# Kernel tuning notes

Measured on AMD Instinct MI355X. Metric: run time of the kernel, lower is better.

Reference implementation:

```python
import jax, jax.numpy as jnp
import numpy as np

B, Tx, H, E, Ky = 64, 128, 1024, 512, 32000


def setup_inputs() -> dict:
    key = jax.random.key(0)
    ks = jax.random.split(key, 14)
    s = 0.02
    return {
        "input": jax.random.randint(ks[0], (B,), 0, Ky),
        "hidden": jax.random.normal(ks[1], (B, H), jnp.float32),
        "enc_output": jax.random.normal(ks[2], (Tx, B, 2 * H), jnp.float32),
        # learned params
        "emb_W": jax.random.normal(ks[3], (Ky, E), jnp.float32) * s,
        "Wih": jax.random.normal(ks[4], (3 * H, E + 2 * H), jnp.float32) * s,
        "Whh": jax.random.normal(ks[5], (3 * H, H), jnp.float32) * s,
        "bih": jax.random.normal(ks[6], (3 * H,), jnp.float32) * s,
        "bhh": jax.random.normal(ks[7], (3 * H,), jnp.float32) * s,
        "lsm_W": jax.random.normal(ks[8], (Ky, 3 * H), jnp.float32) * s,
        "lsm_b": jax.random.normal(ks[9], (Ky,), jnp.float32) * s,
        "aW1": jax.random.normal(ks[10], (H, 3 * H), jnp.float32) * s,
        "ab1": jax.random.normal(ks[11], (H,), jnp.float32) * s,
        "aW2": jax.random.normal(ks[12], (1, H), jnp.float32) * s,
        "ab2": jax.random.normal(ks[13], (1,), jnp.float32) * s,
    }


def _alignment(hidden, enc_output, aW1, ab1, aW2, ab2):
    # hidden [B,H] broadcast over Tx; attn_input [Tx,B,3H]
    Tx_ = enc_output.shape[0]
    h_rep = jnp.broadcast_to(hidden[None], (Tx_,) + hidden.shape)
    attn_in = jnp.concatenate([h_rep, enc_output], axis=2)
    a = jnp.tanh(jnp.einsum('tbi,hi->tbh', attn_in, aW1) + ab1)
    score = jnp.einsum('tbh,oh->tbo', a, aW2) + ab2   # [Tx,B,1]
    w = jax.nn.softmax(score, axis=0)                 # softmax over Tx (dim=0)
    # context = sum_t w[t,b] * enc_output[t,b,:]  -> [B,2H]
    context = jnp.einsum('tb,tbk->bk', w[..., 0], enc_output)
    return context


def _gru_cell(x, h, Wih, Whh, bih, bhh):
    gi = x @ Wih.T + bih   # [B,3H]
    gh = h @ Whh.T + bhh   # [B,3H]
    Hd = h.shape[1]
    i_r, i_z, i_n = gi[:, :Hd], gi[:, Hd:2 * Hd], gi[:, 2 * Hd:]
    h_r, h_z, h_n = gh[:, :Hd], gh[:, Hd:2 * Hd], gh[:, 2 * Hd:]
    r = jax.nn.sigmoid(i_r + h_r)
    z = jax.nn.sigmoid(i_z + h_z)
    n = jnp.tanh(i_n + r * h_n)
    return (1.0 - z) * n + z * h


def reference(input, hidden, enc_output, emb_W, Wih, Whh, bih, bhh,
              lsm_W, lsm_b, aW1, ab1, aW2, ab2):
    context = _alignment(hidden, enc_output, aW1, ab1, aW2, ab2)  # [B,2H]
    embed = emb_W[input]                                          # [B,E]
    rnn_in = jnp.concatenate([embed, context], axis=1)            # [B,E+2H]
    h_new = _gru_cell(rnn_in, hidden, Wih, Whh, bih, bhh)         # [B,H]
    logits = jnp.concatenate([h_new, context], axis=1) @ lsm_W.T + lsm_b
    output = jax.nn.log_softmax(logits, axis=-1)                  # [B,Ky]
    return output, h_new
```

## Files before the change

kernel.cpp:

```cpp
#include <hip/hip_runtime.h>
#include <hip/hip_bf16.h>

#define B_  64
#define TX  128
#define H_  1024
#define E_  512
#define KY  32000
#define H2  2048
#define H3  3072
#define EC  2560
#define M_  (TX*B_)
#define WST 132
#define NS  4

typedef __bf16 bf16x8 __attribute__((ext_vector_type(8)));
typedef unsigned short u16x8 __attribute__((ext_vector_type(8)));
typedef float f32x4 __attribute__((ext_vector_type(4)));

__device__ __forceinline__ unsigned short f2bf(float f) {
  unsigned int u = __builtin_bit_cast(unsigned int, f);
  u += 0x7fff + ((u >> 16) & 1);
  return (unsigned short)(u >> 16);
}

__device__ __forceinline__ void gload16(const void* g, void* l) {
  __builtin_amdgcn_global_load_lds(
      (const __attribute__((address_space(1))) unsigned int*)g,
      (__attribute__((address_space(3))) unsigned int*)l, 16, 0, 0);
}

__global__ void kc_all(const float* __restrict__ enc, const float* __restrict__ aW1,
                       const float* __restrict__ hidden,
                       unsigned short* __restrict__ encb, unsigned short* __restrict__ w1b,
                       unsigned short* __restrict__ hb) {
  size_t gid = (size_t)blockIdx.x * 256 + threadIdx.x;
  if (gid < 2097152) {
    size_t i = gid * 8;
    float4 v0 = *(const float4*)(enc + i);
    float4 v1 = *(const float4*)(enc + i + 4);
    u16x8 o;
    o[0]=f2bf(v0.x); o[1]=f2bf(v0.y); o[2]=f2bf(v0.z); o[3]=f2bf(v0.w);
    o[4]=f2bf(v1.x); o[5]=f2bf(v1.y); o[6]=f2bf(v1.z); o[7]=f2bf(v1.w);
    *(u16x8*)(encb + i) = o;
  } else if (gid < 2359296) {
    size_t idx = (gid - 2097152) * 8;
    int row = (int)(idx >> 11);
    int col = (int)(idx & 2047);
    const float* s = aW1 + (size_t)row * H3 + H_ + col;
    float4 v0 = *(const float4*)(s);
    float4 v1 = *(const float4*)(s + 4);
    u16x8 o;
    o[0]=f2bf(v0.x); o[1]=f2bf(v0.y); o[2]=f2bf(v0.z); o[3]=f2bf(v0.w);
    o[4]=f2bf(v1.x); o[5]=f2bf(v1.y); o[6]=f2bf(v1.z); o[7]=f2bf(v1.w);
    *(u16x8*)(w1b + idx) = o;
  } else {
    size_t idx = (gid - 2359296) * 8;
    if (idx < 65536) {
      float4 v0 = *(const float4*)(hidden + idx);
      float4 v1 = *(const float4*)(hidden + idx + 4);
      u16x8 o;
      o[0]=f2bf(v0.x); o[1]=f2bf(v0.y); o[2]=f2bf(v0.z); o[3]=f2bf(v0.w);
      o[4]=f2bf(v1.x); o[5]=f2bf(v1.y); o[6]=f2bf(v1.z); o[7]=f2bf(v1.w);
      *(u16x8*)(hb + idx) = o;
    }
  }
}

__global__ void k1_hpart(const float* __restrict__ hidden, const float* __restrict__ aW1,
                         const float* __restrict__ ab1, float* __restrict__ hpart) {
  int b = blockIdx.y;
  int wave = threadIdx.x >> 6;
  int lane = threadIdx.x & 63;
  int h = blockIdx.x * 4 + wave;
  const float* wrow = aW1 + (size_t)h * H3;
  const float* hrow = hidden + b * H_;
  float acc = 0.f;
  for (int j = 0; j < H_ / 64; ++j) {
    int i = j * 64 + lane;
    acc += hrow[i] * wrow[i];
  }
  for (int off = 32; off; off >>= 1) acc += __shfl_down(acc, off);
  if (lane == 0) hpart[b * H_ + h] = acc + ab1[h];
}

__global__ __launch_bounds__(256) void k2_mfma(
    const unsigned short* __restrict__ encb, const unsigned short* __restrict__ w1b,
    const float* __restrict__ hpart, const float* __restrict__ aW2,
    float* __restrict__ scorepart) {
  __shared__ __align__(16) unsigned short As[128 * 64];
  __shared__ __align__(16) unsigned short Bs[128 * 64];
  __shared__ float red[128][2];
  int wg = blockIdx.x;
  int swz = (wg & 7) * 64 + (wg >> 3);
  int mt = swz >> 3, nt = swz & 7;
  int m0 = mt * 128, n0 = nt * 128;
  int tid = threadIdx.x;
  int lane = tid & 63, wid = tid >> 6;
  int wr = wid >> 1, wc = wid & 1;
  f32x4 z = {0.f, 0.f, 0.f, 0.f};
  f32x4 acc[4][4];
  #pragma unroll
  for (int i = 0; i < 4; ++i)
    #pragma unroll
    for (int j = 0; j < 4; ++j) acc[i][j] = z;

  int srow = lane >> 3;
  int scol = ((lane & 7) ^ srow) * 8;
  for (int k0 = 0; k0 < H2; k0 += 64) {
    __syncthreads();
    #pragma unroll
    for (int i = 0; i < 4; ++i) {
      int ci = wid * 4 + i;
      int row = ci * 8 + srow;
      gload16(&encb[(size_t)(m0 + row) * H2 + k0 + scol], &As[ci * 512]);
      gload16(&w1b [(size_t)(n0 + row) * H2 + k0 + scol], &Bs[ci * 512]);
    }
    __syncthreads();
    #pragma unroll
    for (int ks = 0; ks < 2; ++ks) {
      bf16x8 af[4], bfr[4];
      #pragma unroll
      for (int i = 0; i < 4; ++i) {
        int ra = wr * 64 + i * 16 + (lane & 15);
        int rb = wc * 64 + i * 16 + (lane & 15);
        int og = (ks * 4 + (lane >> 4));
        af[i]  = *(const bf16x8*)&As[ra * 64 + ((og ^ (ra & 7)) * 8)];
        bfr[i] = *(const bf16x8*)&Bs[rb * 64 + ((og ^ (rb & 7)) * 8)];
      }
      #pragma unroll
      for (int mi = 0; mi < 4; ++mi)
        #pragma unroll
        for (int ni = 0; ni < 4; ++ni)
          acc[mi][ni] = __builtin_amdgcn_mfma_f32_16x16x32_bf16(af[mi], bfr[ni], acc[mi][ni], 0, 0, 0);
    }
  }
  int q = lane >> 4, c = lane & 15;
  #pragma unroll
  for (int mi = 0; mi < 4; ++mi) {
    #pragma unroll
    for (int r = 0; r < 4; ++r) {
      int mloc = wr * 64 + mi * 16 + q * 4 + r;
      int b = (mi * 16 + q * 4 + r) & 63;
      float p = 0.f;
      #pragma unroll
      for (int ni = 0; ni < 4; ++ni) {
        int n = n0 + wc * 64 + ni * 16 + c;
        p += aW2[n] * tanhf(hpart[b * H_ + n] + acc[mi][ni][r]);
      }
      p += __shfl_xor(p, 1); p += __shfl_xor(p, 2);
      p += __shfl_xor(p, 4); p += __shfl_xor(p, 8);
      if (c == 0) red[mloc][wc] = p;
    }
  }
  __syncthreads();
  if (tid < 128)
    scorepart[(size_t)nt * M_ + m0 + tid] = red[tid][0] + red[tid][1];
}

__global__ __launch_bounds__(256) void k2_gemm_score(
    const float* __restrict__ enc, const float* __restrict__ aW1,
    const float* __restrict__ hpart, const float* __restrict__ aW2,
    float* __restrict__ scorepart) {
  __shared__ float As[32][68];
  __shared__ float Bs[32][68];
  __shared__ float red[64][17];
  int m0 = blockIdx.x * 64;
  int n0 = blockIdx.y * 64;
  int tid = threadIdx.x;
  int ty = tid >> 4, tx = tid & 15;
  float acc[4][4] = {};
  for (int k0 = 0; k0 < H2; k0 += 32) {
    #pragma unroll
    for (int l = 0; l < 2; ++l) {
      int fi = tid + l * 256;
      int m = fi >> 3;
      int kq = (fi & 7) * 4;
      const float4 v = *(const float4*)&enc[(size_t)(m0 + m) * H2 + k0 + kq];
      As[kq + 0][m] = v.x; As[kq + 1][m] = v.y; As[kq + 2][m] = v.z; As[kq + 3][m] = v.w;
      const float4 u = *(const float4*)&aW1[(size_t)(n0 + m) * H3 + H_ + k0 + kq];
      Bs[kq + 0][m] = u.x; Bs[kq + 1][m] = u.y; Bs[kq + 2][m] = u.z; Bs[kq + 3][m] = u.w;
    }
    __syncthreads();
    #pragma unroll
    for (int kk = 0; kk < 32; ++kk) {
      float4 av = *(const float4*)&As[kk][ty * 4];
      float4 bv = *(const float4*)&Bs[kk][tx * 4];
      float a[4] = {av.x, av.y, av.z, av.w};
      float b[4] = {bv.x, bv.y, bv.z, bv.w};
      #pragma unroll
      for (int i = 0; i < 4; ++i)
        #pragma unroll
        for (int j = 0; j < 4; ++j)
          acc[i][j] += a[i] * b[j];
    }
    __syncthreads();
  }
  #pragma unroll
  for (int i = 0; i < 4; ++i) {
    int m = m0 + ty * 4 + i;
    int bb = m & 63;
    float p = 0.f;
    #pragma unroll
    for (int j = 0; j < 4; ++j) {
      int n = n0 + tx * 4 + j;
      p += aW2[n] * tanhf(hpart[bb * H_ + n] + acc[i][j]);
    }
    red[ty * 4 + i][tx] = p;
  }
  __syncthreads();
  if (tid < 64) {
    float s = 0.f;
    #pragma unroll
    for (int j = 0; j < 16; ++j) s += red[tid][j];
    scorepart[(size_t)blockIdx.y * M_ + m0 + tid] = s;
  }
}

__global__ void k3_softmax(const float* __restrict__ scorepart, const float* __restrict__ ab2,
                           float* __restrict__ w, int nb) {
  int b = blockIdx.x;
  int t = threadIdx.x;
  float s = ab2[0];
  for (int k = 0; k < nb; ++k) s += scorepart[k * M_ + t * B_ + b];
  __shared__ float sm[128];
  sm[t] = s; __syncthreads();
  for (int off = 64; off; off >>= 1) {
    if (t < off) sm[t] = fmaxf(sm[t], sm[t + off]);
    __syncthreads();
  }
  float mx = sm[0]; __syncthreads();
  float e = expf(s - mx);
  sm[t] = e; __syncthreads();
  for (int off = 64; off; off >>= 1) {
    if (t < off) sm[t] += sm[t + off];
    __syncthreads();
  }
  w[t * B_ + b] = e / sm[0];
}

__global__ __launch_bounds__(256) void k4c_ctx(
    const unsigned short* __restrict__ encb, const float* __restrict__ scorepart,
    const float* __restrict__ ab2, const int* __restrict__ input,
    const float* __restrict__ emb_W, unsigned short* __restrict__ rb,
    unsigned short* __restrict__ xb) {
  int b = blockIdx.y;
  if (blockIdx.x == 4) {
    int tok = input[b];
    for (int c = threadIdx.x; c < E_; c += 256)
      rb[b * EC + c] = f2bf(emb_W[(size_t)tok * E_ + c]);
    return;
  }
  int t = threadIdx.x;
  __shared__ float wl[TX];
  __shared__ float sm[TX];
  float s = 0.f;
  if (t < TX) {
    s = ab2[0];
    #pragma unroll
    for (int k = 0; k < 8; ++k) s += scorepart[k * M_ + t * B_ + b];
    sm[t] = s;
  }
  __syncthreads();
  for (int off = 64; off; off >>= 1) {
    if (t < off) sm[t] = fmaxf(sm[t], sm[t + off]);
    __syncthreads();
  }
  float mx = sm[0]; __syncthreads();
  float e = 0.f;
  if (t < TX) { e = expf(s - mx); sm[t] = e; }
  __syncthreads();
  for (int off = 64; off; off >>= 1) {
    if (t < off) sm[t] += sm[t + off];
    __syncthreads();
  }
  if (t < TX) wl[t] = e / sm[0];
  __syncthreads();

  int kp = blockIdx.x * 256 + threadIdx.x;
  float a0 = 0.f, a1 = 0.f;
  for (int tt = 0; tt < TX; ++tt) {
    unsigned int u = *(const unsigned int*)&encb[((size_t)tt * B_ + b) * H2 + kp * 2];
    float e0 = __builtin_bit_cast(float, u << 16);
    float e1 = __builtin_bit_cast(float, u & 0xffff0000u);
    float wt = wl[tt];
    a0 += wt * e0; a1 += wt * e1;
  }
  unsigned int ob = (unsigned int)f2bf(a0) | ((unsigned int)f2bf(a1) << 16);
  *(unsigned int*)&rb[b * EC + E_ + kp * 2] = ob;
  *(unsigned int*)&xb[b * H3 + H_ + kp * 2] = ob;
}

__global__ void k4_context(const float* __restrict__ enc, const float* __restrict__ w,
                           float* __restrict__ context) {
  int b = blockIdx.y;
  int k = blockIdx.x * 256 + threadIdx.x;
  __shared__ float wl[TX];
  if (threadIdx.x < TX) wl[threadIdx.x] = w[threadIdx.x * B_ + b];
  __syncthreads();
  float acc = 0.f;
  for (int t = 0; t < TX; ++t)
    acc += wl[t] * enc[((size_t)t * B_ + b) * H2 + k];
  context[b * H2 + k] = acc;
}
__global__ void k5a_rnnin(const int* __restrict__ input, const float* __restrict__ emb_W,
                          const float* __restrict__ context, float* __restrict__ rnn_in) {
  int b = blockIdx.x;
  int tok = input[b];
  for (int c = threadIdx.x; c < EC; c += blockDim.x)
    rnn_in[b * EC + c] = (c < E_) ? emb_W[(size_t)tok * E_ + c] : context[b * H2 + (c - E_)];
}

__device__ __forceinline__ void gemmT_body(const float* __restrict__ x,
    const float* __restrict__ W, int lda, const float* __restrict__ bias,
    float* __restrict__ po, int N, int K, int kbeg, int kend, bool addb,
    float* __restrict__ Ws) {
  int tid = threadIdx.x;
  int b = tid & 63, g = tid >> 6;
  int n0 = blockIdx.x * 64;
  float acc[16] = {};
  const float4* xv = (const float4*)(x + (size_t)b * K);
  for (int k0 = kbeg; k0 < kend; k0 += 128) {
    __syncthreads();
    #pragma unroll
    for (int l = 0; l < 8; ++l) {
      int f = l * 256 + tid;
      int row = f >> 5, c4 = f & 31;
      float4 v = *(const float4*)&W[(size_t)(n0 + row) * lda + k0 + c4 * 4];
      *(float4*)&Ws[row * WST + c4 * 4] = v;
    }
    __syncthreads();
    #pragma unroll
    for (int kb = 0; kb < 128; kb += 16) {
      float4 x0 = xv[(k0 + kb) / 4 + 0];
      float4 x1 = xv[(k0 + kb) / 4 + 1];
      float4 x2 = xv[(k0 + kb) / 4 + 2];
      float4 x3 = xv[(k0 + kb) / 4 + 3];
      #pragma unroll
      for (int i = 0; i < 16; ++i) {
        const float* wr = &Ws[(g * 16 + i) * WST + kb];
        float4 w0 = *(const float4*)(wr + 0);
        float4 w1 = *(const float4*)(wr + 4);
        float4 w2 = *(const float4*)(wr + 8);
        float4 w3 = *(const float4*)(wr + 12);
        acc[i] += x0.x*w0.x + x0.y*w0.y + x0.z*w0.z + x0.w*w0.w
                + x1.x*w1.x + x1.y*w1.y + x1.z*w1.z + x1.w*w1.w
                + x2.x*w2.x + x2.y*w2.y + x2.z*w2.z + x2.w*w2.w
                + x3.x*w3.x + x3.y*w3.y + x3.z*w3.z + x3.w*w3.w;
      }
    }
  }
  #pragma unroll
  for (int i = 0; i < 16; ++i) {
    int n = n0 + g * 16 + i;
    float v = acc[i];
    if (addb) v += bias[n];
    po[(size_t)b * N + n] = v;
  }
}

__global__ __launch_bounds__(256) void k_gemm_T(
    const float* __restrict__ x, const float* __restrict__ W,
    const float* __restrict__ bias, float* __restrict__ out, int N, int K) {
  __shared__ float Ws[64 * WST];
  int ks = blockIdx.y;
  int kchunk = K / gridDim.y;
  gemmT_body(x, W, K, bias, out + (size_t)ks * 64 * N, N, K, ks * kchunk, ks * kchunk + kchunk, ks == 0, Ws);
}

__global__ __launch_bounds__(256) void k_gates_mfma(
    const unsigned short* __restrict__ rb, const unsigned short* __restrict__ hb,
    const float* __restrict__ Wih, const float* __restrict__ Whh,
    const float* __restrict__ bih, const float* __restrict__ bhh,
    float* __restrict__ gi, float* __restrict__ gh) {
  __shared__ __align__(16) float Ws[64 * 128];
  __shared__ __align__(16) unsigned short Xs[64 * 128];
  int tid = threadIdx.x;
  int wv = tid >> 6, lane = tid & 63;
  int r = lane & 15, kg = lane >> 4;
  int n0 = blockIdx.x * 64;
  int n = n0 + wv * 16 + r;
  int s = blockIdx.y;
  const float* W; const unsigned short* x; const float* bias;
  float* po; int lda, kbase, KC; bool addb;
  if (s < 2) { W = Wih; x = rb; lda = EC; kbase = s * 1280; KC = 1280;
               po = gi + (size_t)s * B_ * H3; bias = bih; addb = (s == 0); }
  else       { W = Whh; x = hb; lda = H_; kbase = 0; KC = 1024;
               po = gh; bias = bhh; addb = true; }
  f32x4 a0 = {0.f, 0.f, 0.f, 0.f}, a1 = a0, a2 = a0, a3 = a0;

  for (int ch = 0; ch < KC; ch += 128) {
    __syncthreads();
    #pragma unroll
    for (int i = 0; i < 8; ++i) {
      int rowW = (wv * 8 + i) * 2 + (lane >> 5);
      int sc = (lane & 31) ^ (rowW & 15);
      gload16(&W[(size_t)(n0 + rowW) * lda + kbase + ch + sc * 4],
              &Ws[(wv * 8 + i) * 256]);
    }
    #pragma unroll
    for (int i = 0; i < 4; ++i) {
      int rowX = (wv * 4 + i) * 4 + (lane >> 4);
      int sc = (lane & 15) ^ (rowX & 15);
      gload16(&x[(size_t)rowX * lda + kbase + ch + sc * 8],
              &Xs[(wv * 4 + i) * 512]);
    }
    __syncthreads();
    #pragma unroll
    for (int ss = 0; ss < 4; ++ss) {
      int uw0 = (ss * 8 + kg * 2) ^ r;
      int uw1 = (ss * 8 + kg * 2 + 1) ^ r;
      int rw = wv * 16 + r;
      float4 wa = *(const float4*)&Ws[rw * 128 + uw0 * 4];
      float4 wb = *(const float4*)&Ws[rw * 128 + uw1 * 4];
      u16x8 bu;
      bu[0] = f2bf(wa.x); bu[1] = f2bf(wa.y); bu[2] = f2bf(wa.z); bu[3] = f2bf(wa.w);
      bu[4] = f2bf(wb.x); bu[5] = f2bf(wb.y); bu[6] = f2bf(wb.z); bu[7] = f2bf(wb.w);
      bf16x8 bf = __builtin_bit_cast(bf16x8, bu);
      int ux = (ss * 4 + kg) ^ r;
      u16x8 x0 = *(const u16x8*)&Xs[(r)      * 128 + ux * 8];
      u16x8 x1 = *(const u16x8*)&Xs[(16 + r) * 128 + ux * 8];
      u16x8 x2 = *(const u16x8*)&Xs[(32 + r) * 128 + ux * 8];
      u16x8 x3 = *(const u16x8*)&Xs[(48 + r) * 128 + ux * 8];
      a0 = __builtin_amdgcn_mfma_f32_16x16x32_bf16(__builtin_bit_cast(bf16x8, x0), bf, a0, 0, 0, 0);
      a1 = __builtin_amdgcn_mfma_f32_16x16x32_bf16(__builtin_bit_cast(bf16x8, x1), bf, a1, 0, 0, 0);
      a2 = __builtin_amdgcn_mfma_f32_16x16x32_bf16(__builtin_bit_cast(bf16x8, x2), bf, a2, 0, 0, 0);
      a3 = __builtin_amdgcn_mfma_f32_16x16x32_bf16(__builtin_bit_cast(bf16x8, x3), bf, a3, 0, 0, 0);
    }
  }
  float bv = addb ? bias[n] : 0.f;
  int r0 = kg * 4;
  #pragma unroll
  for (int rr = 0; rr < 4; ++rr) {
    po[(size_t)(r0 + rr) * H3 + n]      = a0[rr] + bv;
    po[(size_t)(16 + r0 + rr) * H3 + n] = a1[rr] + bv;
    po[(size_t)(32 + r0 + rr) * H3 + n] = a2[rr] + bv;
    po[(size_t)(48 + r0 + rr) * H3 + n] = a3[rr] + bv;
  }
}

__global__ void k5c_gates(const float* __restrict__ gip, const float* __restrict__ ghp,
                          int gis, int ghs, int do_ctx,
                          const float* __restrict__ hidden, const float* __restrict__ context,
                          float* __restrict__ hnew_out, unsigned short* __restrict__ xb) {
  int b = blockIdx.x;
  for (int h = threadIdx.x; h < H_; h += blockDim.x) {
    float ir = 0.f, iz = 0.f, inn = 0.f;
    for (int s = 0; s < gis; ++s) {
      const float* gb = gip + (size_t)s * B_ * H3 + (size_t)b * H3;
      ir += gb[h]; iz += gb[H_ + h]; inn += gb[H2 + h];
    }
    float hr = 0.f, hz = 0.f, hn = 0.f;
    for (int s = 0; s < ghs; ++s) {
      const float* gb = ghp + (size_t)s * B_ * H3 + (size_t)b * H3;
      hr += gb[h]; hz += gb[H_ + h]; hn += gb[H2 + h];
    }
    float r = 1.f / (1.f + expf(-(ir + hr)));
    float z = 1.f / (1.f + expf(-(iz + hz)));
    float n = tanhf(inn + r * hn);
    float hv = hidden[b * H_ + h];
    float hnew = (1.f - z) * n + z * hv;
    hnew_out[b * H_ + h] = hnew;
    xb[b * H3 + h] = f2bf(hnew);
  }
  if (do_ctx)
    for (int c = threadIdx.x; c < H2; c += blockDim.x)
      xb[b * H3 + H_ + c] = f2bf(context[b * H2 + c]);
}

__device__ __forceinline__ void k6_stage(float4 wa, float4 wb,
    const unsigned short* __restrict__ xp, int off,
    f32x4& a0, f32x4& a1, f32x4& a2, f32x4& a3) {
  u16x8 bu;
  bu[0] = f2bf(wa.x); bu[1] = f2bf(wa.y); bu[2] = f2bf(wa.z); bu[3] = f2bf(wa.w);
  bu[4] = f2bf(wb.x); bu[5] = f2bf(wb.y); bu[6] = f2bf(wb.z); bu[7] = f2bf(wb.w);
  bf16x8 bf = __builtin_bit_cast(bf16x8, bu);
  u16x8 x0 = *(const u16x8*)(xp + off);
  u16x8 x1 = *(const u16x8*)(xp + 16 * H3 + off);
  u16x8 x2 = *(const u16x8*)(xp + 32 * H3 + off);
  u16x8 x3 = *(const u16x8*)(xp + 48 * H3 + off);
  a0 = __builtin_amdgcn_mfma_f32_16x16x32_bf16(__builtin_bit_cast(bf16x8, x0), bf, a0, 0, 0, 0);
  a1 = __builtin_amdgcn_mfma_f32_16x16x32_bf16(__builtin_bit_cast(bf16x8, x1), bf, a1, 0, 0, 0);
  a2 = __builtin_amdgcn_mfma_f32_16x16x32_bf16(__builtin_bit_cast(bf16x8, x2), bf, a2, 0, 0, 0);
  a3 = __builtin_amdgcn_mfma_f32_16x16x32_bf16(__builtin_bit_cast(bf16x8, x3), bf, a3, 0, 0, 0);
}

__global__ __launch_bounds__(256) void k6_split(
    const unsigned short* __restrict__ xb, const float* __restrict__ W,
    float* __restrict__ part) {
  __shared__ __align__(16) float Ws[64 * 128];
  __shared__ __align__(16) unsigned short Xs[64 * 128];
  int tid = threadIdx.x;
  int wv = tid >> 6, lane = tid & 63;
  int r = lane & 15, kg = lane >> 4;
  int n = blockIdx.x * 64 + wv * 16 + r;
  int ks = blockIdx.y;
  const int KC = H3 / NS;
  int kbase = ks * KC;
  f32x4 a0 = {0.f, 0.f, 0.f, 0.f}, a1 = a0, a2 = a0, a3 = a0;

  for (int ch = 0; ch < KC; ch += 128) {
    __syncthreads();
    #pragma unroll
    for (int i = 0; i < 8; ++i) {
      int rowW = (wv * 8 + i) * 2 + (lane >> 5);
      int sc = (lane & 31) ^ (rowW & 15);
      gload16(&W[(size_t)(blockIdx.x * 64 + rowW) * H3 + kbase + ch + sc * 4],
              &Ws[(wv * 8 + i) * 256]);
    }
    #pragma unroll
    for (int i = 0; i < 4; ++i) {
      int rowX = (wv * 4 + i) * 4 + (lane >> 4);
      int sc = (lane & 15) ^ (rowX & 15);
      gload16(&xb[(size_t)rowX * H3 + kbase + ch + sc * 8],
              &Xs[(wv * 4 + i) * 512]);
    }
    __syncthreads();
    #pragma unroll
    for (int s = 0; s < 4; ++s) {
      int uw0 = (s * 8 + kg * 2) ^ r;
      int uw1 = (s * 8 + kg * 2 + 1) ^ r;
      int rw = wv * 16 + r;
      float4 wa = *(const float4*)&Ws[rw * 128 + uw0 * 4];
      float4 wb = *(const float4*)&Ws[rw * 128 + uw1 * 4];
      u16x8 bu;
      bu[0] = f2bf(wa.x); bu[1] = f2bf(wa.y); bu[2] = f2bf(wa.z); bu[3] = f2bf(wa.w);
      bu[4] = f2bf(wb.x); bu[5] = f2bf(wb.y); bu[6] = f2bf(wb.z); bu[7] = f2bf(wb.w);
      bf16x8 bf = __builtin_bit_cast(bf16x8, bu);
      int ux = (s * 4 + kg) ^ r;
      u16x8 x0 = *(const u16x8*)&Xs[(r)      * 128 + ux * 8];
      u16x8 x1 = *(const u16x8*)&Xs[(16 + r) * 128 + ux * 8];
      u16x8 x2 = *(const u16x8*)&Xs[(32 + r) * 128 + ux * 8];
      u16x8 x3 = *(const u16x8*)&Xs[(48 + r) * 128 + ux * 8];
      a0 = __builtin_amdgcn_mfma_f32_16x16x32_bf16(__builtin_bit_cast(bf16x8, x0), bf, a0, 0, 0, 0);
      a1 = __builtin_amdgcn_mfma_f32_16x16x32_bf16(__builtin_bit_cast(bf16x8, x1), bf, a1, 0, 0, 0);
      a2 = __builtin_amdgcn_mfma_f32_16x16x32_bf16(__builtin_bit_cast(bf16x8, x2), bf, a2, 0, 0, 0);
      a3 = __builtin_amdgcn_mfma_f32_16x16x32_bf16(__builtin_bit_cast(bf16x8, x3), bf, a3, 0, 0, 0);
    }
  }
  float* po = part + (size_t)ks * B_ * KY;
  int r0 = kg * 4;
  #pragma unroll
  for (int rr = 0; rr < 4; ++rr) {
    po[(size_t)(r0 + rr) * KY + n]      = a0[rr];
    po[(size_t)(16 + r0 + rr) * KY + n] = a1[rr];
    po[(size_t)(32 + r0 + rr) * KY + n] = a2[rr];
    po[(size_t)(48 + r0 + rr) * KY + n] = a3[rr];
  }
}

__global__ __launch_bounds__(256) void k6_lsm_mfma(
    const unsigned short* __restrict__ xb, const float* __restrict__ W,
    const float* __restrict__ bias, float* __restrict__ out) {
  int tid = threadIdx.x;
  int wv = tid >> 6, lane = tid & 63;
  int n = blockIdx.x * 64 + wv * 16 + (lane & 15);
  int kg = lane >> 4;
  const float* wp = W + (size_t)n * H3 + kg * 8;
  const unsigned short* xp = xb + (size_t)(lane & 15) * H3 + kg * 8;
  f32x4 a0 = {0.f, 0.f, 0.f, 0.f}, a1 = a0, a2 = a0, a3 = a0;
  for (int k0 = 0; k0 < H3; k0 += 128) {
    float4 wA0 = *(const float4*)(wp + k0 +   0);
    float4 wB0 = *(const float4*)(wp + k0 +   4);
    float4 wA1 = *(const float4*)(wp + k0 +  32);
    float4 wB1 = *(const float4*)(wp + k0 +  36);
    float4 wA2 = *(const float4*)(wp + k0 +  64);
    float4 wB2 = *(const float4*)(wp + k0 +  68);
    float4 wA3 = *(const float4*)(wp + k0 +  96);
    float4 wB3 = *(const float4*)(wp + k0 + 100);
    k6_stage(wA0, wB0, xp, k0 +  0, a0, a1, a2, a3);
    k6_stage(wA1, wB1, xp, k0 + 32, a0, a1, a2, a3);
    k6_stage(wA2, wB2, xp, k0 + 64, a0, a1, a2, a3);
    k6_stage(wA3, wB3, xp, k0 + 96, a0, a1, a2, a3);
  }
  float bv = bias[n];
  int r0 = kg * 4;
  #pragma unroll
  for (int r = 0; r < 4; ++r) {
    out[(size_t)(r0 + r) * KY + n]      = a0[r] + bv;
    out[(size_t)(16 + r0 + r) * KY + n] = a1[r] + bv;
    out[(size_t)(32 + r0 + r) * KY + n] = a2[r] + bv;
    out[(size_t)(48 + r0 + r) * KY + n] = a3[r] + bv;
  }
}

__global__ __launch_bounds__(256) void k7a(const float* __restrict__ part,
                                           const float* __restrict__ bias,
                                           float* __restrict__ out,
                                           float* __restrict__ pm, float* __restrict__ ps) {
  int b = blockIdx.y, q = blockIdx.x;
  float* orow = out + (size_t)b * KY;
  int base = q * (KY / 4);
  int end  = base + (KY / 4);
  float mx = -1e30f;
  for (int k = base + threadIdx.x; k < end; k += 256) {
    float v = bias[k];
    #pragma unroll
    for (int s = 0; s < NS; ++s)
      v += part[(size_t)s * B_ * KY + (size_t)b * KY + k];
    orow[k] = v;
    mx = fmaxf(mx, v);
  }
  __shared__ float sm[256];
  sm[threadIdx.x] = mx; __syncthreads();
  for (int off = 128; off; off >>= 1) {
    if (threadIdx.x < off) sm[threadIdx.x] = fmaxf(sm[threadIdx.x], sm[threadIdx.x + off]);
    __syncthreads();
  }
  float M = sm[0]; __syncthreads();
  float s = 0.f;
  for (int k = base + threadIdx.x; k < end; k += 256)
    s += expf(orow[k] - M);
  sm[threadIdx.x] = s; __syncthreads();
  for (int off = 128; off; off >>= 1) {
    if (threadIdx.x < off) sm[threadIdx.x] += sm[threadIdx.x + off];
    __syncthreads();
  }
  if (threadIdx.x == 0) { pm[b * 4 + q] = M; ps[b * 4 + q] = sm[0]; }
}

__global__ void k8f_out(float* __restrict__ outp, const float* __restrict__ pm,
                        const float* __restrict__ ps) {
  int b = blockIdx.y;
  float m0 = pm[b*4], m1 = pm[b*4+1], m2 = pm[b*4+2], m3 = pm[b*4+3];
  float M = fmaxf(fmaxf(m0, m1), fmaxf(m2, m3));
  float s = ps[b*4]   * expf(m0 - M) + ps[b*4+1] * expf(m1 - M)
          + ps[b*4+2] * expf(m2 - M) + ps[b*4+3] * expf(m3 - M);
  float lse = M + logf(s);
  int k = blockIdx.x * 256 + threadIdx.x;
  size_t idx = (size_t)b * KY + k;
  outp[idx] = outp[idx] - lse;
}

__global__ void k7_lse(const float* __restrict__ logits, float* __restrict__ lse) {
  int b = blockIdx.x;
  const float* row = logits + (size_t)b * KY;
  __shared__ float sm[256];
  float mx = -1e30f;
  for (int k = threadIdx.x; k < KY; k += 256) mx = fmaxf(mx, row[k]);
  sm[threadIdx.x] = mx; __syncthreads();
  for (int off = 128; off; off >>= 1) {
    if (threadIdx.x < off) sm[threadIdx.x] = fmaxf(sm[threadIdx.x], sm[threadIdx.x + off]);
    __syncthreads();
  }
  mx = sm[0]; __syncthreads();
  float s = 0.f;
  for (int k = threadIdx.x; k < KY; k += 256) s += expf(row[k] - mx);
  sm[threadIdx.x] = s; __syncthreads();
  for (int off = 128; off; off >>= 1) {
    if (threadIdx.x < off) sm[threadIdx.x] += sm[threadIdx.x + off];
    __syncthreads();
  }
  if (threadIdx.x == 0) lse[b] = mx + logf(sm[0]);
}
__global__ void k8_out(float* __restrict__ outp, const float* __restrict__ lse) {
  int b = blockIdx.y;
  int k = blockIdx.x * 256 + threadIdx.x;
  size_t idx = (size_t)b * KY + k;
  outp[idx] = outp[idx] - lse[b];
}

extern "C" void kernel_launch(void* const* d_in, const int* in_sizes, int n_in,
                              void* d_out, int out_size, void* d_ws, size_t ws_size,
                              hipStream_t stream) {
  const int*   input  = (const int*)  d_in[0];
  const float* hidden = (const float*)d_in[1];
  const float* enc    = (const float*)d_in[2];
  const float* emb_W  = (const float*)d_in[3];
  const float* Wih    = (const float*)d_in[4];
  const float* Whh    = (const float*)d_in[5];
  const float* bih    = (const float*)d_in[6];
  const float* bhh    = (const float*)d_in[7];
  const float* lsm_W  = (const float*)d_in[8];
  const float* lsm_b  = (const float*)d_in[9];
  const float* aW1    = (const float*)d_in[10];
  const float* ab1    = (const float*)d_in[11];
  const float* aW2    = (const float*)d_in[12];
  const float* ab2    = (const float*)d_in[13];

  float* out   = (float*)d_out;
  float* hnew  = out + (size_t)B_ * KY;

  int gis = 5, ghs = 2;
  size_t base_fast = 65536 + 131072 + 8192 + 131072 + 163840
                   + (size_t)gis * 196608 + (size_t)ghs * 196608
                   + 98304 + 64 + 256 + 256 + (size_t)NS * B_ * KY;
  size_t need_fast = (base_fast + 8388608 + 1048576) * 4;
  int fast = (ws_size >= need_fast);
  if (!fast) {
    size_t base_slow = 65536 + 131072 + 8192 + 131072 + 163840
                     + (size_t)gis * 196608 + (size_t)ghs * 196608 + 98304 + 64;
    if (ws_size < base_slow * 4) { gis = 1; ghs = 1; }
  }

  float* ws = (float*)d_ws;
  unsigned short* encb = (unsigned short*)ws;
  unsigned short* w1b  = encb + (fast ? 16777216 : 0);
  float* fbase = fast ? (float*)(w1b + 2097152) : ws;
  float* hpart     = fbase;
  float* scorepart = hpart + 65536;
  float* w         = scorepart + 131072;
  float* context   = w + 8192;
  float* rnn_in    = context + 131072;
  unsigned short* rb = (unsigned short*)rnn_in;
  unsigned short* hb = rb + 163840;
  float* gi        = rnn_in + 163840;
  float* gh        = gi + (size_t)gis * 196608;
  unsigned short* xb = (unsigned short*)(gh + (size_t)ghs * 196608);
  float* lse       = (float*)(xb + 196608);
  float* pm        = lse + 64;
  float* ps        = pm + 256;
  float* part      = ps + 256;

  k1_hpart<<<dim3(256, 64), 256, 0, stream>>>(hidden, aW1, ab1, hpart);
  if (fast) {
    kc_all<<<9248, 256, 0, stream>>>(enc, aW1, hidden, encb, w1b, hb);
    k2_mfma<<<512, 256, 0, stream>>>(encb, w1b, hpart, aW2, scorepart);
    k4c_ctx<<<dim3(5, B_), 256, 0, stream>>>(encb, scorepart, ab2, input, emb_W, rb, xb);
    k_gates_mfma<<<dim3(48, 3), 256, 0, stream>>>(rb, hb, Wih, Whh, bih, bhh, gi, gh);
    k5c_gates<<<B_, 256, 0, stream>>>(gi, gh, 2, 1, 0, hidden, context, hnew, xb);
    k6_split<<<dim3(KY / 64, NS), 256, 0, stream>>>(xb, lsm_W, part);
    k7a<<<dim3(4, B_), 256, 0, stream>>>(part, lsm_b, out, pm, ps);
    k8f_out<<<dim3(KY / 256, B_), 256, 0, stream>>>(out, pm, ps);
  } else {
    k2_gemm_score<<<dim3(M_ / 64, 16), 256, 0, stream>>>(enc, aW1, hpart, aW2, scorepart);
    k3_softmax<<<B_, TX, 0, stream>>>(scorepart, ab2, w, 16);
    k4_context<<<dim3(H2 / 256, B_), 256, 0, stream>>>(enc, w, context);
    k5a_rnnin<<<B_, 256, 0, stream>>>(input, emb_W, context, rnn_in);
    k_gemm_T<<<dim3(H3 / 64, gis), 256, 0, stream>>>(rnn_in, Wih, bih, gi, H3, EC);
    k_gemm_T<<<dim3(H3 / 64, ghs), 256, 0, stream>>>(hidden, Whh, bhh, gh, H3, H_);
    k5c_gates<<<B_, 256, 0, stream>>>(gi, gh, gis, ghs, 1, hidden, context, hnew, xb);
    k6_lsm_mfma<<<KY / 64, 256, 0, stream>>>(xb, lsm_W, lsm_b, out);
    k7_lse<<<B_, 256, 0, stream>>>(out, lse);
    k8_out<<<dim3(KY / 256, B_), 256, 0, stream>>>(out, lse);
  }
}
```

Baseline: 268.0 us.

## Double-buffer k6_split LDS tiles with half-size K chunks

Rewrites the k6_split weight-times-activation loop so that, while the current chunk is consumed by MFMA, the next K chunk is loaded asynchronously into a second shared-memory buffer. The chunk size drops from 128 to 64 and the swizzle and load mapping are adjusted to match, so total LDS use stays the same. The goal is to hide global-load latency behind compute and remove one barrier per iteration. In exchange there are twice as many iterations, and any wait on the async loads before the barrier depends on how gload16 is implemented.

```diff
diff --git a/kernel.cpp b/kernel.cpp
--- a/kernel.cpp
+++ b/kernel.cpp
@@ -487,8 +487,8 @@
 __global__ __launch_bounds__(256) void k6_split(
     const unsigned short* __restrict__ xb, const float* __restrict__ W,
     float* __restrict__ part) {
-  __shared__ __align__(16) float Ws[64 * 128];
-  __shared__ __align__(16) unsigned short Xs[64 * 128];
+  __shared__ __align__(16) float Ws[2][64 * 64];
+  __shared__ __align__(16) unsigned short Xs[2][64 * 64];
   int tid = threadIdx.x;
   int wv = tid >> 6, lane = tid & 63;
   int r = lane & 15, kg = lane >> 4;
@@ -498,45 +498,59 @@
   int kbase = ks * KC;
   f32x4 a0 = {0.f, 0.f, 0.f, 0.f}, a1 = a0, a2 = a0, a3 = a0;
 
-  for (int ch = 0; ch < KC; ch += 128) {
-    __syncthreads();
-    #pragma unroll
-    for (int i = 0; i < 8; ++i) {
-      int rowW = (wv * 8 + i) * 2 + (lane >> 5);
-      int sc = (lane & 31) ^ (rowW & 15);
-      gload16(&W[(size_t)(blockIdx.x * 64 + rowW) * H3 + kbase + ch + sc * 4],
-              &Ws[(wv * 8 + i) * 256]);
-    }
-    #pragma unroll
-    for (int i = 0; i < 4; ++i) {
-      int rowX = (wv * 4 + i) * 4 + (lane >> 4);
-      int sc = (lane & 15) ^ (rowX & 15);
-      gload16(&xb[(size_t)rowX * H3 + kbase + ch + sc * 8],
-              &Xs[(wv * 4 + i) * 512]);
-    }
-    __syncthreads();
-    #pragma unroll
-    for (int s = 0; s < 4; ++s) {
-      int uw0 = (s * 8 + kg * 2) ^ r;
-      int uw1 = (s * 8 + kg * 2 + 1) ^ r;
-      int rw = wv * 16 + r;
-      float4 wa = *(const float4*)&Ws[rw * 128 + uw0 * 4];
-      float4 wb = *(const float4*)&Ws[rw * 128 + uw1 * 4];
+  int wRow0 = lane >> 4;
+  int wUnit = lane & 15;
+  int xRow0 = lane >> 3;
+  int xUnit = lane & 7;
+
+#define K6_STAGE(BUF, CH)                                                         \
+  {                                                                               \
+    _Pragma("unroll")                                                             \
+    for (int i = 0; i < 4; ++i) {                                                 \
+      int rowW = (wv * 4 + i) * 4 + wRow0;                                        \
+      int sc = wUnit ^ (rowW & 15);                                               \
+      gload16(&W[(size_t)(blockIdx.x * 64 + rowW) * H3 + kbase + (CH) + sc * 4],  \
+              &Ws[BUF][(wv * 4 + i) * 256]);                                      \
+    }                                                                             \
+    _Pragma("unroll")                                                             \
+    for (int i = 0; i < 2; ++i) {                                                 \
+      int rowX = (wv * 2 + i) * 8 + xRow0;                                        \
+      int sc = xUnit ^ (rowX & 7);                                                \
+      gload16(&xb[(size_t)rowX * H3 + kbase + (CH) + sc * 8],                     \
+              &Xs[BUF][(wv * 2 + i) * 512]);                                      \
+    }                                                                             \
+  }
+
+  K6_STAGE(0, 0);
+  __syncthreads();
+  int buf = 0;
+  for (int ch = 0; ch < KC; ch += 64) {
+    if (ch + 64 < KC) K6_STAGE(buf ^ 1, ch + 64);
+    int rw = wv * 16 + r;
+    #pragma unroll
+    for (int ss = 0; ss < 2; ++ss) {
+      int uw0 = (ss * 8 + kg * 2) ^ r;
+      int uw1 = (ss * 8 + kg * 2 + 1) ^ r;
+      float4 wa = *(const float4*)&Ws[buf][rw * 64 + uw0 * 4];
+      float4 wb = *(const float4*)&Ws[buf][rw * 64 + uw1 * 4];
       u16x8 bu;
       bu[0] = f2bf(wa.x); bu[1] = f2bf(wa.y); bu[2] = f2bf(wa.z); bu[3] = f2bf(wa.w);
       bu[4] = f2bf(wb.x); bu[5] = f2bf(wb.y); bu[6] = f2bf(wb.z); bu[7] = f2bf(wb.w);
       bf16x8 bf = __builtin_bit_cast(bf16x8, bu);
-      int ux = (s * 4 + kg) ^ r;
-      u16x8 x0 = *(const u16x8*)&Xs[(r)      * 128 + ux * 8];
-      u16x8 x1 = *(const u16x8*)&Xs[(16 + r) * 128 + ux * 8];
-      u16x8 x2 = *(const u16x8*)&Xs[(32 + r) * 128 + ux * 8];
-      u16x8 x3 = *(const u16x8*)&Xs[(48 + r) * 128 + ux * 8];
+      int ux = (ss * 4 + kg) ^ (r & 7);
+      u16x8 x0 = *(const u16x8*)&Xs[buf][(r)      * 64 + ux * 8];
+      u16x8 x1 = *(const u16x8*)&Xs[buf][(16 + r) * 64 + ux * 8];
+      u16x8 x2 = *(const u16x8*)&Xs[buf][(32 + r) * 64 + ux * 8];
+      u16x8 x3 = *(const u16x8*)&Xs[buf][(48 + r) * 64 + ux * 8];
       a0 = __builtin_amdgcn_mfma_f32_16x16x32_bf16(__builtin_bit_cast(bf16x8, x0), bf, a0, 0, 0, 0);
       a1 = __builtin_amdgcn_mfma_f32_16x16x32_bf16(__builtin_bit_cast(bf16x8, x1), bf, a1, 0, 0, 0);
       a2 = __builtin_amdgcn_mfma_f32_16x16x32_bf16(__builtin_bit_cast(bf16x8, x2), bf, a2, 0, 0, 0);
       a3 = __builtin_amdgcn_mfma_f32_16x16x32_bf16(__builtin_bit_cast(bf16x8, x3), bf, a3, 0, 0, 0);
     }
-  }
+    __syncthreads();
+    buf ^= 1;
+  }
+#undef K6_STAGE
   float* po = part + (size_t)ks * B_ * KY;
   int r0 = kg * 4;
   #pragma unroll
```

Result: no change. 273.1 us (+1.9%).
